# Performance work log

Hardware: AMD Instinct MI355X
Metric: run time of the kernel (lower is better)

## Reference

```python
import jax, jax.numpy as jnp
import numpy as np

MUL_SRC = 64
MUL_DST = 16
N_PATHS = 3  # l = 0, 1, 2 (parities e,o,e match SH 0e,1o,2e)
SQ3 = 3.0 ** 0.5
SQ5 = 5.0 ** 0.5
SQ15 = 15.0 ** 0.5


def spherical_harmonics_l012(vec):
    """Real SH (component normalization, e3nn ordering) of normalized vec. [E,3]->[E,9]."""
    r = vec / jnp.maximum(jnp.linalg.norm(vec, axis=-1, keepdims=True), 1e-9)
    x, y, z = r[:, 0], r[:, 1], r[:, 2]
    sh0 = jnp.ones_like(x)
    return jnp.stack([
        sh0,
        SQ3 * x, SQ3 * y, SQ3 * z,
        SQ15 * x * y, SQ15 * y * z, 0.5 * SQ5 * (3.0 * z * z - 1.0),
        SQ15 * x * z, 0.5 * SQ15 * (x * x - y * y),
    ], axis=-1)


def setup_inputs() -> dict:
    key = jax.random.key(0)
    ks = jax.random.split(key, 8)
    n_src, n_dst, E = 10000, 10000, 50000
    esd, hidden = 32, 128
    wnumel = MUL_SRC * MUL_DST * N_PATHS  # 3072
    return {
        "h_src": jax.random.normal(ks[0], (n_src, MUL_SRC), jnp.float32),
        "edge_vec": jax.random.normal(ks[1], (E, 3), jnp.float32),
        "edge_scalars": jax.random.normal(ks[2], (E, esd), jnp.float32),
        "W1": jax.random.normal(ks[3], (esd, hidden), jnp.float32) / np.sqrt(esd),
        "b1": jnp.zeros((hidden,), jnp.float32),
        "W2": jax.random.normal(ks[4], (hidden, wnumel), jnp.float32) / np.sqrt(hidden),
        "b2": jnp.zeros((wnumel,), jnp.float32),
        "src_idx": jax.random.randint(ks[5], (E,), 0, n_src),
        "dst_idx": jax.random.randint(ks[6], (E,), 0, n_dst),
        "n_dst": n_dst,
    }


def reference(h_src, edge_vec, edge_scalars, W1, b1, W2, b2, src_idx, dst_idx, n_dst):
    E = edge_vec.shape[0]
    # 1) spherical harmonics of edge directions: [E, 9]
    sh = spherical_harmonics_l012(edge_vec)
    # 2) edge-conditioned TP weights via MLP: [E, 3*64*16]
    w = jax.nn.silu(edge_scalars @ W1 + b1) @ W2 + b2
    w = w.reshape(E, N_PATHS, MUL_SRC, MUL_DST)
    # 3) gather source scalars and contract per path: 0e x l -> l (CG is identity)
    x = h_src[src_idx]  # [E, 64]
    feat = jnp.einsum("eu,eluv->elv", x, w) / np.sqrt(MUL_SRC)  # [E, 3, 16]
    # 4) outer product with SH per l, mul_ir layout: [E, 16*(2l+1)] blocks
    sh_l = (sh[:, 0:1], sh[:, 1:4], sh[:, 4:9])
    msg = jnp.concatenate(
        [(feat[:, l, :, None] * sh_l[l][:, None, :]).reshape(E, -1) for l in range(N_PATHS)],
        axis=-1,
    )  # [E, 144]
    # 5) scatter-mean over destination nodes
    seg = jax.ops.segment_sum(msg, dst_idx, num_segments=n_dst)
    cnt = jax.ops.segment_sum(jnp.ones((E,), msg.dtype), dst_idx, num_segments=n_dst)
    return seg / jnp.maximum(cnt, 1.0)[:, None]
```

## Files before the change

### kernel.cpp

```cpp
#include <hip/hip_runtime.h>
#include <hip/hip_bf16.h>

typedef unsigned short u16;
typedef __attribute__((ext_vector_type(8))) short short8;
typedef __attribute__((ext_vector_type(4))) float f32x4;

#define HID 128
#define WNUMEL 3072
#define OUTD 144

__global__ void k_pre(const float* __restrict__ W2, __hip_bfloat16* __restrict__ W2s,
                      const float* __restrict__ es, const float* __restrict__ W1,
                      const float* __restrict__ b1, __hip_bfloat16* __restrict__ h2s,
                      const float* __restrict__ ev, const int* __restrict__ dst,
                      float* __restrict__ shb, int* __restrict__ head,
                      int* __restrict__ nxt, int E, int NW, int NM) {
  __shared__ u16 wlds[4096];
  const int b = blockIdx.x, tid = threadIdx.x;
  if (b < NW) {
    int f = b * 256 + tid;
    int k = f / WNUMEL, n = f - k * WNUMEL;
    int s = k >> 5, h = (k >> 3) & 3, i = k & 7;
    int tt = n >> 4, c = n & 15;
    W2s[((size_t)(tt * 4 + s) * 64 + (c + 16 * h)) * 8 + i] = __float2bfloat16(W2[f]);
  } else if (b < NW + NM) {
    const int e0 = (b - NW) * 64;
    const int w = tid >> 6, l = tid & 63;
    const int c = l & 15, kb = 8 * ((l >> 4) & 3);
#pragma unroll
    for (int q = 0; q < 2; ++q) {
      int nt = 2 * w + q;
      int n = nt * 16 + c;
#pragma unroll
      for (int i = 0; i < 8; ++i)
        wlds[(nt * 64 + l) * 8 + i] = (u16)__bfloat16_as_ushort(
            __float2bfloat16(W1[(kb + i) * HID + n]));
    }
    short8 ef = {0, 0, 0, 0, 0, 0, 0, 0};
    {
      int e = e0 + w * 16 + c;
      if (e < E) {
        const float4 p0 = *(const float4*)(es + (size_t)e * 32 + kb);
        const float4 p1 = *(const float4*)(es + (size_t)e * 32 + kb + 4);
        u16* pe = (u16*)&ef;
#pragma unroll
        for (int i = 0; i < 4; ++i) {
          pe[i]     = __bfloat16_as_ushort(__float2bfloat16((&p0.x)[i]));
          pe[4 + i] = __bfloat16_as_ushort(__float2bfloat16((&p1.x)[i]));
        }
      }
    }
    __syncthreads();
#pragma unroll
    for (int nt = 0; nt < 8; ++nt) {
      short8 bf = *(const short8*)(wlds + (nt * 64 + l) * 8);
      float b1v = b1[nt * 16 + c];
      f32x4 acc = {b1v, b1v, b1v, b1v};
      acc = __builtin_amdgcn_mfma_f32_16x16x32_bf16(ef, bf, acc, 0, 0, 0);
      int hh = (2 * nt + (c >> 3)) & 3;
      int s = nt >> 1;
      int i = c & 7;
#pragma unroll
      for (int j = 0; j < 4; ++j) {
        int e = e0 + w * 16 + (l >> 4) * 4 + j;
        if (e < E) {
          float a = acc[j];
          float z = a / (1.f + expf(-a)) * 0.125f;
          h2s[((size_t)(e >> 4) * 4 + s) * 512 + ((e & 15) + 16 * hh) * 8 + i] =
              __float2bfloat16(z);
        }
      }
    }
  } else {
    int e = (b - NW - NM) * 256 + tid;
    if (e >= E) return;
    float vx = ev[e * 3 + 0], vy = ev[e * 3 + 1], vz = ev[e * 3 + 2];
    float nrm = fmaxf(sqrtf(vx * vx + vy * vy + vz * vz), 1e-9f);
    float x = vx / nrm, y = vy / nrm, z = vz / nrm;
    const float SQ3 = 1.7320508075688772f, SQ5 = 2.2360679774997896f,
                SQ15 = 3.872983346207417f;
    float* sp = shb + (size_t)e * 9;
    sp[0] = 1.f;
    sp[1] = SQ3 * x; sp[2] = SQ3 * y; sp[3] = SQ3 * z;
    sp[4] = SQ15 * x * y; sp[5] = SQ15 * y * z;
    sp[6] = 0.5f * SQ5 * (3.f * z * z - 1.f);
    sp[7] = SQ15 * x * z;
    sp[8] = 0.5f * SQ15 * (x * x - y * y);
    nxt[e] = atomicExch(&head[dst[e]], e);
  }
}

__global__ __launch_bounds__(256, 2) void k_gemm(
    const u16* __restrict__ h2s, const u16* __restrict__ W2s,
    const float* __restrict__ hsrc, const int* __restrict__ srci,
    const float* __restrict__ b2, float* __restrict__ feat_out, int E) {
  __shared__ float lds[4160];
  float* xT = lds;
  float* fl = lds;
  const int tid = threadIdx.x, lane = tid & 63, wave = tid >> 6;
  const int blk = blockIdx.x, l3 = blockIdx.y;
  const int c = lane & 15, g = lane >> 4;

  {
    int e = lane, u0 = wave * 16;
    int eg = min(blk * 64 + e, E - 1);
    const float* xr = hsrc + (size_t)srci[eg] * 64 + u0;
#pragma unroll
    for (int k = 0; k < 16; ++k) xT[(u0 + k) * 64 + e] = xr[k];
  }
  short8 af[4][4];
#pragma unroll
  for (int mt = 0; mt < 4; ++mt)
#pragma unroll
    for (int s = 0; s < 4; ++s)
      af[mt][s] = *(const short8*)(h2s + ((size_t)((blk * 4 + mt) * 4 + s) * 64 + lane) * 8);
  __syncthreads();

  float feat[4][4] = {};
  const int T0 = l3 * 64 + wave * 16;
  const u16* Bg = W2s + (size_t)T0 * 2048;
  const float* b2g = b2 + T0 * 16 + c;

#pragma unroll
  for (int k = 0; k < 16; ++k) {
    short8 bf[4];
#pragma unroll
    for (int s = 0; s < 4; ++s)
      bf[s] = *(const short8*)(Bg + ((size_t)(k * 4 + s) * 64 + lane) * 8);
    float b2v = 0.125f * b2g[k * 16];
#pragma unroll
    for (int mt = 0; mt < 4; ++mt) {
      f32x4 acc = {b2v, b2v, b2v, b2v};
#pragma unroll
      for (int s = 0; s < 4; ++s)
        acc = __builtin_amdgcn_mfma_f32_16x16x32_bf16(af[mt][s], bf[s], acc, 0, 0, 0);
      const float4 xv = *(const float4*)&xT[(wave * 16 + k) * 64 + mt * 16 + g * 4];
#pragma unroll
      for (int j = 0; j < 4; ++j)
        feat[mt][j] = fmaf((&xv.x)[j], acc[j], feat[mt][j]);
    }
  }

  __syncthreads();
#pragma unroll
  for (int mt = 0; mt < 4; ++mt)
#pragma unroll
    for (int j = 0; j < 4; ++j)
      fl[wave * 1040 + (mt * 16 + g * 4 + j) * 16 + c] = feat[mt][j];
  __syncthreads();

#pragma unroll
  for (int r = 0; r < 4; ++r) {
    int p = r * 256 + tid;
    int eloc = p >> 4, v = p & 15;
    float f = fl[p] + fl[1040 + p] + fl[2080 + p] + fl[3120 + p];
    int e = blk * 64 + eloc;
    if (e < E) feat_out[(size_t)e * 48 + l3 * 16 + v] = f;
  }
}

__global__ void k_gather(const float* __restrict__ feat, const float* __restrict__ shb,
                         const int* __restrict__ head, const int* __restrict__ nxt,
                         float* __restrict__ out, int n_dst) {
  int d = blockIdx.x * 4 + (threadIdx.x >> 6);
  int lane = threadIdx.x & 63;
  if (d >= n_dst) return;
  int fi[4], si[4];
#pragma unroll
  for (int r = 0; r < 4; ++r) {
    int o = lane * 4 + r;
    if (o < 16)      { fi[r] = o;                 si[r] = 0; }
    else if (o < 64) { int id = o - 16; fi[r] = 16 + id / 3; si[r] = 1 + id % 3; }
    else             { int id = o - 64; fi[r] = 32 + id / 5; si[r] = 4 + id % 5; }
  }
  int e = head[d];
  float4 acc = {0.f, 0.f, 0.f, 0.f};
  int deg = 0;
  while (e >= 0) {
    int en = nxt[e];
    if (lane < 36) {
      const float* fp = feat + (size_t)e * 48;
      const float* sp = shb + (size_t)e * 9;
#pragma unroll
      for (int r = 0; r < 4; ++r)
        (&acc.x)[r] = fmaf(fp[fi[r]], sp[si[r]], (&acc.x)[r]);
    }
    ++deg;
    e = en;
  }
  if (lane < 36) {
    float inv = 1.f / (float)max(deg, 1);
    acc.x *= inv; acc.y *= inv; acc.z *= inv; acc.w *= inv;
    *(float4*)&out[(size_t)d * OUTD + lane * 4] = acc;
  }
}

extern "C" void kernel_launch(void* const* d_in, const int* in_sizes, int n_in,
                              void* d_out, int out_size, void* d_ws, size_t ws_size,
                              hipStream_t stream) {
  const float* h_src        = (const float*)d_in[0];
  const float* edge_vec     = (const float*)d_in[1];
  const float* edge_scalars = (const float*)d_in[2];
  const float* W1           = (const float*)d_in[3];
  const float* b1           = (const float*)d_in[4];
  const float* W2           = (const float*)d_in[5];
  const float* b2           = (const float*)d_in[6];
  const int*   src_idx      = (const int*)d_in[7];
  const int*   dst_idx      = (const int*)d_in[8];

  const int E = in_sizes[1] / 3;
  const int n_dst = out_size / OUTD;
  const int nblk64 = (E + 63) / 64;
  const size_t E_pad = (size_t)nblk64 * 64;

  char* w = (char*)d_ws;
  auto al = [](size_t x) { return (x + 255) & ~(size_t)255; };
  size_t o = 0;
  float* shb = (float*)(w + o);                   o += al(E_pad * 9 * 4);
  __hip_bfloat16* h2s = (__hip_bfloat16*)(w + o); o += al(E_pad * 128 * 2);
  __hip_bfloat16* W2s = (__hip_bfloat16*)(w + o); o += al((size_t)128 * 3072 * 2);
  float* featb = (float*)(w + o);                 o += al(E_pad * 48 * 4);
  int* head  = (int*)(w + o);                     o += al((size_t)n_dst * 4);
  int* nxt   = (int*)(w + o);                     o += al((size_t)E * 4);

  hipMemsetAsync(head, 0xFF, (size_t)n_dst * 4, stream);

  const int NW = (128 * WNUMEL) / 256;
  const int NM = (E + 63) / 64;
  const int NL = (E + 255) / 256;
  k_pre<<<NW + NM + NL, 256, 0, stream>>>(W2, W2s, edge_scalars, W1, b1, h2s,
                                          edge_vec, dst_idx, shb, head, nxt, E, NW, NM);
  dim3 gg(nblk64, 3);
  k_gemm<<<gg, 256, 0, stream>>>((const u16*)h2s, (const u16*)W2s, h_src, src_idx,
                                 b2, featb, E);
  k_gather<<<(n_dst + 3) / 4, 256, 0, stream>>>(featb, shb, head, nxt,
                                                (float*)d_out, n_dst);
}
```

Measured before the change: 79.62 us.

## Vectorize W2 and h2s packing stores and use 16 lanes per node in gather

The W2 conversion now has each thread pack 8 bf16 values into one 16-byte store, which cuts that block count by 8x. The layer-1 MFMA swaps its operand order so each lane holds 4 consecutive hidden units and writes them as one 8-byte store instead of scattered 2-byte stores. The gather kernel assigns 16 threads per destination node, each handling 9 outputs, where before a 64-lane wave left 28 lanes idle. This raises lane utilization but makes the output stores and feature loads scalar and strided.

```diff
diff --git a/kernel.cpp b/kernel.cpp
--- a/kernel.cpp
+++ b/kernel.cpp
@@ -2,6 +2,7 @@
 #include <hip/hip_bf16.h>
 
 typedef unsigned short u16;
+typedef __attribute__((ext_vector_type(4))) short short4v;
 typedef __attribute__((ext_vector_type(8))) short short8;
 typedef __attribute__((ext_vector_type(4))) float f32x4;
 
@@ -18,57 +19,60 @@
   __shared__ u16 wlds[4096];
   const int b = blockIdx.x, tid = threadIdx.x;
   if (b < NW) {
-    int f = b * 256 + tid;
-    int k = f / WNUMEL, n = f - k * WNUMEL;
-    int s = k >> 5, h = (k >> 3) & 3, i = k & 7;
-    int tt = n >> 4, c = n & 15;
-    W2s[((size_t)(tt * 4 + s) * 64 + (c + 16 * h)) * 8 + i] = __float2bfloat16(W2[f]);
+    int t = b * 256 + tid;
+    int kh = t / WNUMEL, n = t - kh * WNUMEL;
+    int s = kh >> 2, h = kh & 3, tt = n >> 4, c = n & 15;
+    short8 pk;
+#pragma unroll
+    for (int i = 0; i < 8; ++i)
+      ((u16*)&pk)[i] = __bfloat16_as_ushort(
+          __float2bfloat16(W2[(size_t)(8 * kh + i) * WNUMEL + n]));
+    *(short8*)(W2s + ((size_t)(tt * 4 + s) * 64 + (c + 16 * h)) * 8) = pk;
   } else if (b < NW + NM) {
     const int e0 = (b - NW) * 64;
     const int w = tid >> 6, l = tid & 63;
-    const int c = l & 15, kb = 8 * ((l >> 4) & 3);
+    const int c = l & 15, g = l >> 4;
+    const int kb = 8 * g;
 #pragma unroll
     for (int q = 0; q < 2; ++q) {
       int nt = 2 * w + q;
       int n = nt * 16 + c;
 #pragma unroll
       for (int i = 0; i < 8; ++i)
-        wlds[(nt * 64 + l) * 8 + i] = (u16)__bfloat16_as_ushort(
-            __float2bfloat16(W1[(kb + i) * HID + n]));
+        wlds[(nt * 64 + l) * 8 + i] = __bfloat16_as_ushort(
+            __float2bfloat16(W1[(size_t)(kb + i) * HID + n]));
     }
     short8 ef = {0, 0, 0, 0, 0, 0, 0, 0};
-    {
-      int e = e0 + w * 16 + c;
+    const int e = e0 + w * 16 + c;
+    if (e < E) {
+      const float4 p0 = *(const float4*)(es + (size_t)e * 32 + kb);
+      const float4 p1 = *(const float4*)(es + (size_t)e * 32 + kb + 4);
+#pragma unroll
+      for (int i = 0; i < 4; ++i) {
+        ((u16*)&ef)[i]     = __bfloat16_as_ushort(__float2bfloat16((&p0.x)[i]));
+        ((u16*)&ef)[4 + i] = __bfloat16_as_ushort(__float2bfloat16((&p1.x)[i]));
+      }
+    }
+    __syncthreads();
+#pragma unroll
+    for (int nt = 0; nt < 8; ++nt) {
+      short8 wf = *(const short8*)(wlds + (nt * 64 + l) * 8);
+      const float4 b1q = *(const float4*)(b1 + nt * 16 + g * 4);
+      f32x4 acc = {b1q.x, b1q.y, b1q.z, b1q.w};
+      acc = __builtin_amdgcn_mfma_f32_16x16x32_bf16(wf, ef, acc, 0, 0, 0);
       if (e < E) {
-        const float4 p0 = *(const float4*)(es + (size_t)e * 32 + kb);
-        const float4 p1 = *(const float4*)(es + (size_t)e * 32 + kb + 4);
-        u16* pe = (u16*)&ef;
-#pragma unroll
-        for (int i = 0; i < 4; ++i) {
-          pe[i]     = __bfloat16_as_ushort(__float2bfloat16((&p0.x)[i]));
-          pe[4 + i] = __bfloat16_as_ushort(__float2bfloat16((&p1.x)[i]));
-        }
-      }
-    }
-    __syncthreads();
-#pragma unroll
-    for (int nt = 0; nt < 8; ++nt) {
-      short8 bf = *(const short8*)(wlds + (nt * 64 + l) * 8);
-      float b1v = b1[nt * 16 + c];
-      f32x4 acc = {b1v, b1v, b1v, b1v};
-      acc = __builtin_amdgcn_mfma_f32_16x16x32_bf16(ef, bf, acc, 0, 0, 0);
-      int hh = (2 * nt + (c >> 3)) & 3;
-      int s = nt >> 1;
-      int i = c & 7;
-#pragma unroll
-      for (int j = 0; j < 4; ++j) {
-        int e = e0 + w * 16 + (l >> 4) * 4 + j;
-        if (e < E) {
+        int s = nt >> 1;
+        int hh = (2 * nt + (g >> 1)) & 3;
+        int i0 = 4 * (g & 1);
+        short4v pk;
+#pragma unroll
+        for (int j = 0; j < 4; ++j) {
           float a = acc[j];
           float z = a / (1.f + expf(-a)) * 0.125f;
-          h2s[((size_t)(e >> 4) * 4 + s) * 512 + ((e & 15) + 16 * hh) * 8 + i] =
-              __float2bfloat16(z);
+          ((u16*)&pk)[j] = __bfloat16_as_ushort(__float2bfloat16(z));
         }
+        *(short4v*)(h2s + ((size_t)(e >> 4) * 4 + s) * 512 +
+                    ((e & 15) + 16 * hh) * 8 + i0) = pk;
       }
     }
   } else {
@@ -162,37 +166,35 @@
 __global__ void k_gather(const float* __restrict__ feat, const float* __restrict__ shb,
                          const int* __restrict__ head, const int* __restrict__ nxt,
                          float* __restrict__ out, int n_dst) {
-  int d = blockIdx.x * 4 + (threadIdx.x >> 6);
-  int lane = threadIdx.x & 63;
+  const int tid = threadIdx.x;
+  const int d = blockIdx.x * 16 + (tid >> 4);
+  const int q = tid & 15;
   if (d >= n_dst) return;
-  int fi[4], si[4];
-#pragma unroll
-  for (int r = 0; r < 4; ++r) {
-    int o = lane * 4 + r;
+  int fi[9], si[9];
+#pragma unroll
+  for (int r = 0; r < 9; ++r) {
+    int o = q * 9 + r;
     if (o < 16)      { fi[r] = o;                 si[r] = 0; }
     else if (o < 64) { int id = o - 16; fi[r] = 16 + id / 3; si[r] = 1 + id % 3; }
     else             { int id = o - 64; fi[r] = 32 + id / 5; si[r] = 4 + id % 5; }
   }
   int e = head[d];
-  float4 acc = {0.f, 0.f, 0.f, 0.f};
+  float acc[9] = {};
   int deg = 0;
   while (e >= 0) {
     int en = nxt[e];
-    if (lane < 36) {
-      const float* fp = feat + (size_t)e * 48;
-      const float* sp = shb + (size_t)e * 9;
-#pragma unroll
-      for (int r = 0; r < 4; ++r)
-        (&acc.x)[r] = fmaf(fp[fi[r]], sp[si[r]], (&acc.x)[r]);
-    }
+    const float* fp = feat + (size_t)e * 48;
+    const float* sp = shb + (size_t)e * 9;
+#pragma unroll
+    for (int r = 0; r < 9; ++r)
+      acc[r] = fmaf(fp[fi[r]], sp[si[r]], acc[r]);
     ++deg;
     e = en;
   }
-  if (lane < 36) {
-    float inv = 1.f / (float)max(deg, 1);
-    acc.x *= inv; acc.y *= inv; acc.z *= inv; acc.w *= inv;
-    *(float4*)&out[(size_t)d * OUTD + lane * 4] = acc;
-  }
+  const float inv = 1.f / (float)max(deg, 1);
+  float* ob = out + (size_t)d * OUTD + q * 9;
+#pragma unroll
+  for (int r = 0; r < 9; ++r) ob[r] = acc[r] * inv;
 }
 
 extern "C" void kernel_launch(void* const* d_in, const int* in_sizes, int n_in,
@@ -225,7 +227,7 @@
 
   hipMemsetAsync(head, 0xFF, (size_t)n_dst * 4, stream);
 
-  const int NW = (128 * WNUMEL) / 256;
+  const int NW = (16 * WNUMEL) / 256;
   const int NM = (E + 63) / 64;
   const int NL = (E + 255) / 256;
   k_pre<<<NW + NM + NL, 256, 0, stream>>>(W2, W2s, edge_scalars, W1, b1, h2s,
@@ -233,6 +235,6 @@
   dim3 gg(nblk64, 3);
   k_gemm<<<gg, 256, 0, stream>>>((const u16*)h2s, (const u16*)W2s, h_src, src_idx,
                                  b2, featb, E);
-  k_gather<<<(n_dst + 3) / 4, 256, 0, stream>>>(featb, shb, head, nxt,
-                                                (float*)d_out, n_dst);
-}
+  k_gather<<<(n_dst + 15) / 16, 256, 0, stream>>>(featb, shb, head, nxt,
+                                                  (float*)d_out, n_dst);
+}
```

New measurement: 83.02 us. +4.3%, slower.
